# Kernel optimization log

Hardware: AMD Instinct MI355X
Metric: run time of the kernel (lower is better)

The kernel has to match this reference:

```python
import jax, jax.numpy as jnp
import numpy as np

# RosaAttention config constants
H = 16       # num_rosa_heads
KV = 4       # num_rosa_key_value_heads
QKB = 64     # num_rosa_query_key_bits
VB = 64      # num_rosa_value_bits
HID = 2048   # hidden_size
TAU = 1.0    # temperature buffer


def setup_inputs() -> dict:
    key = jax.random.key(0)
    ks = jax.random.split(key, 8)
    B, S = 2, 2048
    sc = 0.02
    return {
        "x": jax.random.normal(ks[0], (B, S, HID), jnp.float32),
        "attention_mask": jnp.ones((B, S), jnp.int32),
        "Wq": jax.random.normal(ks[1], (HID, H * QKB), jnp.float32) * sc,
        "Wk": jax.random.normal(ks[2], (HID, KV * QKB), jnp.float32) * sc,
        "Wv": jax.random.normal(ks[3], (HID, KV * VB), jnp.float32) * sc,
        "Wo": jax.random.normal(ks[4], (H * VB, HID), jnp.float32) * sc,
        "emb0": jnp.full((H, VB), -1e-05, jnp.float32),
        "emb1": jnp.full((H, VB), +1e-05, jnp.float32),
    }


def reference(x, attention_mask, Wq, Wk, Wv, Wo, emb0, emb1):
    B, S, _ = x.shape
    rep = H // KV
    # projections -> [b, s, heads, bits]
    xq = (x @ Wq).reshape(B, S, H, QKB)
    xk = (x @ Wk).reshape(B, S, KV, QKB)
    xv = (x @ Wv).reshape(B, S, KV, VB)
    # repeat_kv: each kv head repeated n_rep times contiguously
    xk = jnp.repeat(xk, rep, axis=2)   # [b, s, H, QKB]
    xv = jnp.repeat(xv, rep, axis=2)   # [b, s, H, VB]
    # soft bit quantization of q/k, tau-scaled bit-similarity score
    qb = jnp.tanh(xq)
    kb = jnp.tanh(xk)
    scores = jnp.einsum('bqhd,bkhd->bhqk', qb, kb) / (TAU * QKB)
    # causal mask + padding mask (mask True = attend)
    causal = jnp.tril(jnp.ones((S, S), bool))
    mask = causal[None, None] & attention_mask.astype(bool)[:, None, None, :]
    scores = jnp.where(mask, scores, jnp.finfo(scores.dtype).min)
    probs = jax.nn.softmax(scores, axis=-1)        # [b, h, q, k]
    # soft-binarized values: per-bit probabilities, attended, then mapped
    # through learned per-head bit embeddings emb0 (bit=0) / emb1 (bit=1)
    vp = jax.nn.sigmoid(xv)                        # [b, s, H, VB]
    ctx = jnp.einsum('bhqk,bkhv->bqhv', probs, vp) # [b, s, H, VB]
    out_bits = ctx * emb1[None, None] + (1.0 - ctx) * emb0[None, None]
    out = out_bits.reshape(B, S, H * VB) @ Wo      # [b, s, HID]
    return out
```

## Files before the change

### kernel.cpp

```cpp
#include <hip/hip_runtime.h>
#include <math.h>

typedef short bf16x8 __attribute__((ext_vector_type(8)));
typedef float f32x4 __attribute__((ext_vector_type(4)));

#define MFMA_BF16(A,B,C) __builtin_amdgcn_mfma_f32_16x16x32_bf16(A,B,C,0,0,0)

__device__ __forceinline__ unsigned short f2b(float x) {
    union { float f; unsigned int u; } v; v.f = x;
    unsigned int r = v.u + 0x7FFFu + ((v.u >> 16) & 1u);
    return (unsigned short)(r >> 16);
}

__device__ __forceinline__ void gload16(const unsigned short* g, unsigned short* l) {
    __builtin_amdgcn_global_load_lds(
        (const __attribute__((address_space(1))) unsigned int*)(g),
        (__attribute__((address_space(3))) unsigned int*)(l),
        16, 0, 0);
}
__device__ __forceinline__ void gload4(const int* g, int* l) {
    __builtin_amdgcn_global_load_lds(
        (const __attribute__((address_space(1))) unsigned int*)(g),
        (__attribute__((address_space(3))) unsigned int*)(l),
        4, 0, 0);
}

__global__ __launch_bounds__(256) void conv_bf16(const float* __restrict__ s,
                                                 unsigned short* __restrict__ d, int n)
{
    int i = blockIdx.x * blockDim.x + threadIdx.x;
    int stride = gridDim.x * blockDim.x;
    for (int idx = i * 4; idx < n; idx += stride * 4) {
        float4 v = *(const float4*)(s + idx);
        ushort4 o;
        o.x = f2b(v.x); o.y = f2b(v.y); o.z = f2b(v.z); o.w = f2b(v.w);
        *(ushort4*)(d + idx) = o;
    }
}

__global__ __launch_bounds__(256) void transp_conv_qkv(const float* __restrict__ Wq,
                                                       const float* __restrict__ Wk,
                                                       const float* __restrict__ Wv,
                                                       unsigned short* __restrict__ dst)
{
    __shared__ float t[32][33];
    const int tx = threadIdx.x, ty = threadIdx.y;
    int bx = blockIdx.x;
    const float* src; int C, cb, dco;
    if (bx < 32)      { src = Wq; C = 1024; cb = bx;      dco = 0; }
    else if (bx < 40) { src = Wk; C = 256;  cb = bx - 32; dco = 1024; }
    else              { src = Wv; C = 256;  cb = bx - 40; dco = 1280; }
    const int c = cb * 32 + tx;
    const int r0 = blockIdx.y * 32;
#pragma unroll
    for (int i = 0; i < 4; ++i)
        t[ty + i * 8][tx] = src[(size_t)(r0 + ty + i * 8) * C + c];
    __syncthreads();
    const int cc = cb * 32 + ty;
#pragma unroll
    for (int i = 0; i < 4; ++i)
        dst[(size_t)(dco + cc + i * 8) * 2048 + r0 + tx] = f2b(t[tx][ty + i * 8]);
}

__global__ __launch_bounds__(256) void transp_conv(const float* __restrict__ src, int R, int C,
                                                   unsigned short* __restrict__ dst, int pitch)
{
    __shared__ float t[32][33];
    const int tx = threadIdx.x, ty = threadIdx.y;
    const int c = blockIdx.x * 32 + tx;
    const int r0 = blockIdx.y * 32;
#pragma unroll
    for (int i = 0; i < 4; ++i)
        t[ty + i * 8][tx] = src[(size_t)(r0 + ty + i * 8) * C + c];
    __syncthreads();
    const int cc = blockIdx.x * 32 + ty;
#pragma unroll
    for (int i = 0; i < 4; ++i)
        dst[(size_t)(cc + i * 8) * pitch + r0 + tx] = f2b(t[tx][ty + i * 8]);
}

template <int MODE>
__global__ __launch_bounds__(256, 3) void gemm_bt_mfma(
    const unsigned short* __restrict__ A,
    const unsigned short* __restrict__ Bt,
    int M, int N, int K,
    float* __restrict__ Cf,
    unsigned short* __restrict__ qh,
    unsigned short* __restrict__ kh,
    unsigned short* __restrict__ vtt)
{
    __shared__ __align__(16) unsigned short As[2][2 * 128 * 32];
    __shared__ __align__(16) unsigned short Bs[2][2 * 64 * 32];

    const int tid = threadIdx.x;
    const int w = tid >> 6, lane = tid & 63, l15 = lane & 15, quad = lane >> 4;
    const int wm = w & 1, wn = w >> 1;
    const int m0 = blockIdx.y * 128, n0 = blockIdx.x * 64;

    f32x4 acc[4][2];
    const f32x4 zero4 = {0.f, 0.f, 0.f, 0.f};
#pragma unroll
    for (int i = 0; i < 4; ++i)
#pragma unroll
        for (int j = 0; j < 2; ++j) acc[i][j] = zero4;

    const int lrow = lane >> 2, lcol = (lane & 3) * 8;
    const unsigned short* AgL = A  + (size_t)(m0 + w * 32 + lrow) * K + lcol;
    const unsigned short* BgL = Bt + (size_t)(n0 + w * 16 + lrow) * K + lcol;

#pragma unroll
    for (int t = 0; t < 4; ++t) {
        const int sub = t >> 1, half = t & 1;
        gload16(AgL + (size_t)(half * 16) * K + sub * 32,
                &As[0][sub * 4096 + (w * 32 + half * 16) * 32]);
    }
#pragma unroll
    for (int kk = 0; kk < 2; ++kk)
        gload16(BgL + kk * 32, &Bs[0][kk * 2048 + (w * 16) * 32]);
    __syncthreads();

    int cb = 0;
    for (int k0 = 0; k0 < K; k0 += 64) {
        if (k0 + 64 < K) {
            const int nb = cb ^ 1;
#pragma unroll
            for (int t = 0; t < 4; ++t) {
                const int sub = t >> 1, half = t & 1;
                gload16(AgL + (size_t)(half * 16) * K + (k0 + 64) + sub * 32,
                        &As[nb][sub * 4096 + (w * 32 + half * 16) * 32]);
            }
#pragma unroll
            for (int kk = 0; kk < 2; ++kk)
                gload16(BgL + (k0 + 64) + kk * 32, &Bs[nb][kk * 2048 + (w * 16) * 32]);
        }

        bf16x8 af[4][2], bf[2][2];
#pragma unroll
        for (int kk = 0; kk < 2; ++kk) {
#pragma unroll
            for (int mt = 0; mt < 4; ++mt)
                af[mt][kk] = *(const bf16x8*)&As[cb][kk * 4096 + (wm * 64 + mt * 16 + l15) * 32 + quad * 8];
#pragma unroll
            for (int nt = 0; nt < 2; ++nt)
                bf[nt][kk] = *(const bf16x8*)&Bs[cb][kk * 2048 + (wn * 32 + nt * 16 + l15) * 32 + quad * 8];
        }
#pragma unroll
        for (int kk = 0; kk < 2; ++kk)
#pragma unroll
            for (int mt = 0; mt < 4; ++mt)
#pragma unroll
                for (int nt = 0; nt < 2; ++nt)
                    acc[mt][nt] = MFMA_BF16(af[mt][kk], bf[nt][kk], acc[mt][nt]);

        __syncthreads();
        cb ^= 1;
    }

    if (MODE == 0) {
#pragma unroll
        for (int mt = 0; mt < 4; ++mt)
#pragma unroll
            for (int nt = 0; nt < 2; ++nt) {
                const int gn = n0 + wn * 32 + nt * 16 + l15;
#pragma unroll
                for (int r = 0; r < 4; ++r) {
                    const int gm = m0 + wm * 64 + mt * 16 + quad * 4 + r;
                    Cf[(size_t)gm * N + gn] = acc[mt][nt][r];
                }
            }
    } else {
        if (n0 < 1024) {
#pragma unroll
            for (int mt = 0; mt < 4; ++mt)
#pragma unroll
                for (int nt = 0; nt < 2; ++nt) {
                    const int gn = n0 + wn * 32 + nt * 16 + l15;
#pragma unroll
                    for (int r = 0; r < 4; ++r) {
                        const int gm = m0 + wm * 64 + mt * 16 + quad * 4 + r;
                        qh[(size_t)gm * 1024 + gn] = f2b(tanhf(acc[mt][nt][r]));
                    }
                }
        } else if (n0 < 1280) {
#pragma unroll
            for (int mt = 0; mt < 4; ++mt)
#pragma unroll
                for (int nt = 0; nt < 2; ++nt) {
                    const int gn = n0 + wn * 32 + nt * 16 + l15 - 1024;
#pragma unroll
                    for (int r = 0; r < 4; ++r) {
                        const int gm = m0 + wm * 64 + mt * 16 + quad * 4 + r;
                        kh[(size_t)gm * 256 + gn] = f2b(tanhf(acc[mt][nt][r]));
                    }
                }
        } else {
#pragma unroll
            for (int mt = 0; mt < 4; ++mt)
#pragma unroll
                for (int nt = 0; nt < 2; ++nt) {
                    const int gn = n0 + wn * 32 + nt * 16 + l15 - 1280;
                    const int g = gn >> 6, vv = gn & 63;
                    const int s0 = m0 + wm * 64 + mt * 16 + quad * 4;
                    const int b = s0 >> 11, sl = s0 & 2047;
                    ushort4 pk;
                    unsigned short* pp = (unsigned short*)&pk;
#pragma unroll
                    for (int r = 0; r < 4; ++r) {
                        float sv = 1.0f / (1.0f + __expf(-acc[mt][nt][r]));
                        pp[r] = f2b(sv);
                    }
                    *(ushort4*)&vtt[((size_t)(b * 4 + g) * 64 + vv) * 2048 + sl] = pk;
                }
        }
    }
}

__global__ __launch_bounds__(256) void rosa_attn_mfma(
    const unsigned short* __restrict__ qh,
    const unsigned short* __restrict__ kh,
    const unsigned short* __restrict__ vtt,
    const int* __restrict__ amask,
    const float* __restrict__ emb0,
    const float* __restrict__ emb1,
    unsigned short* __restrict__ ob)
{
    __shared__ __align__(16) unsigned short Ks[2][2][64 * 32];
    __shared__ __align__(16) unsigned short Vs[2][2][64 * 32];
    __shared__ __align__(16) unsigned short Ps[4][16][72];
    __shared__ int Mski[2][64];

    const int pairI = blockIdx.x;
    const int h = blockIdx.y, b = blockIdx.z, g = h >> 2;
    const int tid = threadIdx.x;
    const int w = tid >> 6, lane = tid & 63, l15 = lane & 15, quad = lane >> 4;

    const int lrow = lane >> 2, lcol = (lane & 3) * 8;
    const unsigned short* kst = kh + (size_t)b * 2048 * 256 + g * 64
                               + (size_t)(w * 16 + lrow) * 256 + lcol;
    const unsigned short* vst = vtt + ((size_t)(b * 4 + g) * 64) * 2048
                               + (size_t)(w * 16 + lrow) * 2048 + lcol;
    const int* mbase = amask + b * 2048;

    const f32x4 zero4 = {0.f, 0.f, 0.f, 0.f};
    const float cexp = 0.0225421100f;

#define STAGE_TILE(k0s, buf)                                              \
    {                                                                     \
        gload16(kst + (size_t)(k0s) * 256,      &Ks[buf][0][(w * 16) * 32]); \
        gload16(kst + (size_t)(k0s) * 256 + 32, &Ks[buf][1][(w * 16) * 32]); \
        gload16(vst + (k0s),                    &Vs[buf][0][(w * 16) * 32]); \
        gload16(vst + (k0s) + 32,               &Vs[buf][1][(w * 16) * 32]); \
        if (w == 0) gload4(mbase + (k0s) + lane, &Mski[buf][0]);          \
    }

    for (int half = 0; half < 2; ++half) {
        const int qt = (half == 0) ? pairI : 31 - pairI;
        const int q0 = qt * 64;
        const int nkt = qt + 1;
        const int qg = q0 + w * 16 + l15;

        const unsigned short* qrow = qh + ((size_t)(b * 2048 + q0 + w * 16 + l15) * 16 + h) * 64;
        const bf16x8 qf0 = *(const bf16x8*)(qrow + quad * 8);
        const bf16x8 qf1 = *(const bf16x8*)(qrow + 32 + quad * 8);

        f32x4 oacc[4];
#pragma unroll
        for (int t = 0; t < 4; ++t) oacc[t] = zero4;
        float psum = 0.0f;

        __syncthreads();
        STAGE_TILE(0, 0)
        __syncthreads();

        int cb = 0;
        for (int kt = 0; kt < nkt; ++kt) {
            if (kt + 1 < nkt) STAGE_TILE((kt + 1) * 64, cb ^ 1)

            const int k0 = kt * 64;
            const bool diag = (kt == qt);
            const int ntlim = diag ? (w + 1) : 4;

#pragma unroll
            for (int nt = 0; nt < 4; ++nt) {
                ushort4 pk;
                if (nt < ntlim) {
                    bf16x8 kf0 = *(const bf16x8*)&Ks[cb][0][(nt * 16 + l15) * 32 + quad * 8];
                    bf16x8 kf1 = *(const bf16x8*)&Ks[cb][1][(nt * 16 + l15) * 32 + quad * 8];
                    f32x4 sc = MFMA_BF16(kf0, qf0, zero4);
                    sc = MFMA_BF16(kf1, qf1, sc);
                    const int4 m4 = *(const int4*)&Mski[cb][nt * 16 + quad * 4];
                    const int* mm = (const int*)&m4;
                    unsigned short* pp = (unsigned short*)&pk;
#pragma unroll
                    for (int r = 0; r < 4; ++r) {
                        float p = __builtin_exp2f(sc[r] * cexp);
                        bool valid = (mm[r] != 0);
                        if (diag) valid = valid && ((k0 + nt * 16 + quad * 4 + r) <= qg);
                        p = valid ? p : 0.0f;
                        psum += p;
                        pp[r] = f2b(p);
                    }
                } else {
                    pk.x = 0; pk.y = 0; pk.z = 0; pk.w = 0;
                }
                *(ushort4*)&Ps[w][l15][nt * 16 + quad * 4] = pk;
            }

            const bf16x8 pf0 = *(const bf16x8*)&Ps[w][l15][quad * 8];
            const bf16x8 pf1 = *(const bf16x8*)&Ps[w][l15][32 + quad * 8];
#pragma unroll
            for (int nt = 0; nt < 4; ++nt) {
                bf16x8 vf0 = *(const bf16x8*)&Vs[cb][0][(nt * 16 + l15) * 32 + quad * 8];
                bf16x8 vf1 = *(const bf16x8*)&Vs[cb][1][(nt * 16 + l15) * 32 + quad * 8];
                oacc[nt] = MFMA_BF16(pf0, vf0, oacc[nt]);
                oacc[nt] = MFMA_BF16(pf1, vf1, oacc[nt]);
            }

            if (kt + 1 < nkt) {
                __syncthreads();
                cb ^= 1;
            }
        }

        float l = psum;
        l += __shfl_xor(l, 16);
        l += __shfl_xor(l, 32);
        float lq[4];
#pragma unroll
        for (int r = 0; r < 4; ++r) lq[r] = __shfl(l, quad * 4 + r);

#pragma unroll
        for (int nt = 0; nt < 4; ++nt) {
            const float e0 = emb0[h * 64 + nt * 16 + l15];
            const float e1 = emb1[h * 64 + nt * 16 + l15];
#pragma unroll
            for (int r = 0; r < 4; ++r) {
                const float ctx = oacc[nt][r] / lq[r];
                const float val = e0 + ctx * (e1 - e0);
                const size_t s_idx = (size_t)(b * 2048 + q0 + w * 16 + quad * 4 + r);
                ob[(s_idx * 16 + h) * 64 + nt * 16 + l15] = f2b(val);
            }
        }
    }
#undef STAGE_TILE
}

extern "C" void kernel_launch(void* const* d_in, const int* in_sizes, int n_in,
                              void* d_out, int out_size, void* d_ws, size_t ws_size,
                              hipStream_t stream)
{
    const float* x    = (const float*)d_in[0];
    const int*   amask= (const int*)d_in[1];
    const float* Wq   = (const float*)d_in[2];
    const float* Wk   = (const float*)d_in[3];
    const float* Wv   = (const float*)d_in[4];
    const float* Wo   = (const float*)d_in[5];
    const float* emb0 = (const float*)d_in[6];
    const float* emb1 = (const float*)d_in[7];
    float* out = (float*)d_out;

    char* base = (char*)d_ws;
    unsigned short* xh    = (unsigned short*)(base);
    unsigned short* ob    = xh;
    unsigned short* Wqkvt = (unsigned short*)(base + (16u << 20));
    unsigned short* Wot   = (unsigned short*)(base + (22u << 20));
    unsigned short* qh    = (unsigned short*)(base + (26u << 20));
    unsigned short* kh    = (unsigned short*)(base + (34u << 20));
    unsigned short* vtt   = (unsigned short*)(base + (36u << 20));

    conv_bf16<<<2048, 256, 0, stream>>>(x, xh, 4096 * 2048);
    transp_conv_qkv<<<dim3(48, 64), dim3(32, 8), 0, stream>>>(Wq, Wk, Wv, Wqkvt);
    transp_conv<<<dim3(64, 32), dim3(32, 8), 0, stream>>>(Wo, 1024, 2048, Wot, 1024);

    gemm_bt_mfma<1><<<dim3(24, 32), 256, 0, stream>>>(xh, Wqkvt, 4096, 1536, 2048,
                                                      nullptr, qh, kh, vtt);
    rosa_attn_mfma<<<dim3(16, 16, 2), 256, 0, stream>>>(qh, kh, vtt, amask, emb0, emb1, ob);
    gemm_bt_mfma<0><<<dim3(32, 32), 256, 0, stream>>>(ob, Wot, 4096, 2048, 1024,
                                                      out, nullptr, nullptr, nullptr);
}
```

Before: 235.0 us.

## Use fragment-major LDS layout, split attention query tiles across blocks, pack bf16 via cvt_pk

LDS tiles in the GEMM and attention kernels are now stored in MFMA fragment order, so each lane reads its 16 bytes contiguously (lane*8) instead of striding by rows. This is meant to remove LDS bank conflicts on fragment loads. The attention kernel now launches one block per query tile, ordered longest-first, instead of pairing short and long tiles in one block, and adds launch_bounds occupancy 3. Probability packing uses the hardware v_cvt_pk_bf16_f32 instruction instead of manual rounding, and the diagonal causal check is simplified to a single tile. Per-block work becomes uneven, which the reversed tile order is meant to offset.

```diff
diff --git a/kernel.cpp b/kernel.cpp
--- a/kernel.cpp
+++ b/kernel.cpp
@@ -3,6 +3,8 @@
 
 typedef short bf16x8 __attribute__((ext_vector_type(8)));
 typedef float f32x4 __attribute__((ext_vector_type(4)));
+typedef unsigned int u32x2 __attribute__((ext_vector_type(2)));
+typedef unsigned int u32x4 __attribute__((ext_vector_type(4)));
 
 #define MFMA_BF16(A,B,C) __builtin_amdgcn_mfma_f32_16x16x32_bf16(A,B,C,0,0,0)
 
@@ -10,6 +12,12 @@
     union { float f; unsigned int u; } v; v.f = x;
     unsigned int r = v.u + 0x7FFFu + ((v.u >> 16) & 1u);
     return (unsigned short)(r >> 16);
+}
+
+__device__ __forceinline__ unsigned int cvtpk(float lo, float hi) {
+    unsigned int r;
+    asm("v_cvt_pk_bf16_f32 %0, %1, %2" : "=v"(r) : "v"(lo), "v"(hi));
+    return r;
 }
 
 __device__ __forceinline__ void gload16(const unsigned short* g, unsigned short* l) {
@@ -104,19 +112,18 @@
 #pragma unroll
         for (int j = 0; j < 2; ++j) acc[i][j] = zero4;
 
-    const int lrow = lane >> 2, lcol = (lane & 3) * 8;
-    const unsigned short* AgL = A  + (size_t)(m0 + w * 32 + lrow) * K + lcol;
-    const unsigned short* BgL = Bt + (size_t)(n0 + w * 16 + lrow) * K + lcol;
+    const unsigned short* AgL = A  + (size_t)(m0 + w * 32 + l15) * K + quad * 8;
+    const unsigned short* BgL = Bt + (size_t)(n0 + w * 16 + l15) * K + quad * 8;
 
 #pragma unroll
     for (int t = 0; t < 4; ++t) {
         const int sub = t >> 1, half = t & 1;
         gload16(AgL + (size_t)(half * 16) * K + sub * 32,
-                &As[0][sub * 4096 + (w * 32 + half * 16) * 32]);
+                &As[0][sub * 4096 + (w * 2 + half) * 512]);
     }
 #pragma unroll
     for (int kk = 0; kk < 2; ++kk)
-        gload16(BgL + kk * 32, &Bs[0][kk * 2048 + (w * 16) * 32]);
+        gload16(BgL + kk * 32, &Bs[0][kk * 2048 + w * 512]);
     __syncthreads();
 
     int cb = 0;
@@ -127,11 +134,11 @@
             for (int t = 0; t < 4; ++t) {
                 const int sub = t >> 1, half = t & 1;
                 gload16(AgL + (size_t)(half * 16) * K + (k0 + 64) + sub * 32,
-                        &As[nb][sub * 4096 + (w * 32 + half * 16) * 32]);
+                        &As[nb][sub * 4096 + (w * 2 + half) * 512]);
             }
 #pragma unroll
             for (int kk = 0; kk < 2; ++kk)
-                gload16(BgL + (k0 + 64) + kk * 32, &Bs[nb][kk * 2048 + (w * 16) * 32]);
+                gload16(BgL + (k0 + 64) + kk * 32, &Bs[nb][kk * 2048 + w * 512]);
         }
 
         bf16x8 af[4][2], bf[2][2];
@@ -139,10 +146,10 @@
         for (int kk = 0; kk < 2; ++kk) {
 #pragma unroll
             for (int mt = 0; mt < 4; ++mt)
-                af[mt][kk] = *(const bf16x8*)&As[cb][kk * 4096 + (wm * 64 + mt * 16 + l15) * 32 + quad * 8];
+                af[mt][kk] = *(const bf16x8*)&As[cb][kk * 4096 + (wm * 4 + mt) * 512 + lane * 8];
 #pragma unroll
             for (int nt = 0; nt < 2; ++nt)
-                bf[nt][kk] = *(const bf16x8*)&Bs[cb][kk * 2048 + (wn * 32 + nt * 16 + l15) * 32 + quad * 8];
+                bf[nt][kk] = *(const bf16x8*)&Bs[cb][kk * 2048 + (wn * 2 + nt) * 512 + lane * 8];
         }
 #pragma unroll
         for (int kk = 0; kk < 2; ++kk)
@@ -215,7 +222,7 @@
     }
 }
 
-__global__ __launch_bounds__(256) void rosa_attn_mfma(
+__global__ __launch_bounds__(256, 3) void rosa_attn_mfma(
     const unsigned short* __restrict__ qh,
     const unsigned short* __restrict__ kh,
     const unsigned short* __restrict__ vtt,
@@ -224,122 +231,119 @@
     const float* __restrict__ emb1,
     unsigned short* __restrict__ ob)
 {
-    __shared__ __align__(16) unsigned short Ks[2][2][64 * 32];
-    __shared__ __align__(16) unsigned short Vs[2][2][64 * 32];
-    __shared__ __align__(16) unsigned short Ps[4][16][72];
+    __shared__ __align__(16) unsigned short Ks[2][2][2048];
+    __shared__ __align__(16) unsigned short Vs[2][2][2048];
+    __shared__ __align__(16) unsigned int   Ps[4][16][36];
     __shared__ int Mski[2][64];
 
-    const int pairI = blockIdx.x;
+    const int qt = 31 - blockIdx.x;
     const int h = blockIdx.y, b = blockIdx.z, g = h >> 2;
     const int tid = threadIdx.x;
     const int w = tid >> 6, lane = tid & 63, l15 = lane & 15, quad = lane >> 4;
 
-    const int lrow = lane >> 2, lcol = (lane & 3) * 8;
     const unsigned short* kst = kh + (size_t)b * 2048 * 256 + g * 64
-                               + (size_t)(w * 16 + lrow) * 256 + lcol;
-    const unsigned short* vst = vtt + ((size_t)(b * 4 + g) * 64) * 2048
-                               + (size_t)(w * 16 + lrow) * 2048 + lcol;
+                               + (size_t)(w * 16 + l15) * 256 + quad * 8;
+    const unsigned short* vst = vtt + ((size_t)(b * 4 + g) * 64 + w * 16 + l15) * 2048
+                               + quad * 8;
     const int* mbase = amask + b * 2048;
 
     const f32x4 zero4 = {0.f, 0.f, 0.f, 0.f};
     const float cexp = 0.0225421100f;
 
-#define STAGE_TILE(k0s, buf)                                              \
-    {                                                                     \
-        gload16(kst + (size_t)(k0s) * 256,      &Ks[buf][0][(w * 16) * 32]); \
-        gload16(kst + (size_t)(k0s) * 256 + 32, &Ks[buf][1][(w * 16) * 32]); \
-        gload16(vst + (k0s),                    &Vs[buf][0][(w * 16) * 32]); \
-        gload16(vst + (k0s) + 32,               &Vs[buf][1][(w * 16) * 32]); \
-        if (w == 0) gload4(mbase + (k0s) + lane, &Mski[buf][0]);          \
-    }
-
-    for (int half = 0; half < 2; ++half) {
-        const int qt = (half == 0) ? pairI : 31 - pairI;
-        const int q0 = qt * 64;
-        const int nkt = qt + 1;
-        const int qg = q0 + w * 16 + l15;
-
-        const unsigned short* qrow = qh + ((size_t)(b * 2048 + q0 + w * 16 + l15) * 16 + h) * 64;
-        const bf16x8 qf0 = *(const bf16x8*)(qrow + quad * 8);
-        const bf16x8 qf1 = *(const bf16x8*)(qrow + 32 + quad * 8);
-
-        f32x4 oacc[4];
-#pragma unroll
-        for (int t = 0; t < 4; ++t) oacc[t] = zero4;
-        float psum = 0.0f;
-
-        __syncthreads();
-        STAGE_TILE(0, 0)
-        __syncthreads();
-
-        int cb = 0;
-        for (int kt = 0; kt < nkt; ++kt) {
-            if (kt + 1 < nkt) STAGE_TILE((kt + 1) * 64, cb ^ 1)
-
-            const int k0 = kt * 64;
-            const bool diag = (kt == qt);
-            const int ntlim = diag ? (w + 1) : 4;
-
-#pragma unroll
-            for (int nt = 0; nt < 4; ++nt) {
-                ushort4 pk;
-                if (nt < ntlim) {
-                    bf16x8 kf0 = *(const bf16x8*)&Ks[cb][0][(nt * 16 + l15) * 32 + quad * 8];
-                    bf16x8 kf1 = *(const bf16x8*)&Ks[cb][1][(nt * 16 + l15) * 32 + quad * 8];
-                    f32x4 sc = MFMA_BF16(kf0, qf0, zero4);
-                    sc = MFMA_BF16(kf1, qf1, sc);
-                    const int4 m4 = *(const int4*)&Mski[cb][nt * 16 + quad * 4];
-                    const int* mm = (const int*)&m4;
-                    unsigned short* pp = (unsigned short*)&pk;
-#pragma unroll
-                    for (int r = 0; r < 4; ++r) {
-                        float p = __builtin_exp2f(sc[r] * cexp);
-                        bool valid = (mm[r] != 0);
-                        if (diag) valid = valid && ((k0 + nt * 16 + quad * 4 + r) <= qg);
-                        p = valid ? p : 0.0f;
-                        psum += p;
-                        pp[r] = f2b(p);
-                    }
-                } else {
-                    pk.x = 0; pk.y = 0; pk.z = 0; pk.w = 0;
-                }
-                *(ushort4*)&Ps[w][l15][nt * 16 + quad * 4] = pk;
+#define STAGE_TILE(k0s, buf)                                               \
+    {                                                                      \
+        gload16(kst + (size_t)(k0s) * 256,      &Ks[buf][0][w * 512]);     \
+        gload16(kst + (size_t)(k0s) * 256 + 32, &Ks[buf][1][w * 512]);     \
+        gload16(vst + (k0s),                    &Vs[buf][0][w * 512]);     \
+        gload16(vst + (k0s) + 32,               &Vs[buf][1][w * 512]);     \
+        if (w == 0) gload4(mbase + (k0s) + lane, &Mski[buf][0]);           \
+    }
+
+    const int q0 = qt * 64;
+    const int nkt = qt + 1;
+    const int qg = q0 + w * 16 + l15;
+
+    const unsigned short* qrow = qh + ((size_t)(b * 2048 + qg) * 16 + h) * 64;
+    const bf16x8 qf0 = *(const bf16x8*)(qrow + quad * 8);
+    const bf16x8 qf1 = *(const bf16x8*)(qrow + 32 + quad * 8);
+
+    f32x4 oacc[4];
+#pragma unroll
+    for (int t = 0; t < 4; ++t) oacc[t] = zero4;
+    float psum = 0.0f;
+
+    STAGE_TILE(0, 0)
+    __syncthreads();
+
+    int cb = 0;
+    for (int kt = 0; kt < nkt; ++kt) {
+        if (kt + 1 < nkt) STAGE_TILE((kt + 1) * 64, cb ^ 1)
+
+        const bool diag = (kt == qt);
+        const int ntlim = diag ? (w + 1) : 4;
+
+#pragma unroll
+        for (int nt = 0; nt < 4; ++nt) {
+            u32x2 pk2;
+            if (nt < ntlim) {
+                bf16x8 kf0 = *(const bf16x8*)&Ks[cb][0][nt * 512 + lane * 8];
+                bf16x8 kf1 = *(const bf16x8*)&Ks[cb][1][nt * 512 + lane * 8];
+                f32x4 sc = MFMA_BF16(kf0, qf0, zero4);
+                sc = MFMA_BF16(kf1, qf1, sc);
+                const int4 m4 = *(const int4*)&Mski[cb][nt * 16 + quad * 4];
+                const int* mm = (const int*)&m4;
+                const bool dnw = diag && (nt == w);
+                float p[4];
+#pragma unroll
+                for (int r = 0; r < 4; ++r) {
+                    float pv = __builtin_exp2f(sc[r] * cexp);
+                    bool valid = (mm[r] != 0);
+                    if (dnw) valid = valid && ((quad * 4 + r) <= l15);
+                    pv = valid ? pv : 0.0f;
+                    psum += pv;
+                    p[r] = pv;
+                }
+                pk2[0] = cvtpk(p[0], p[1]);
+                pk2[1] = cvtpk(p[2], p[3]);
+            } else {
+                pk2[0] = 0u; pk2[1] = 0u;
             }
-
-            const bf16x8 pf0 = *(const bf16x8*)&Ps[w][l15][quad * 8];
-            const bf16x8 pf1 = *(const bf16x8*)&Ps[w][l15][32 + quad * 8];
-#pragma unroll
-            for (int nt = 0; nt < 4; ++nt) {
-                bf16x8 vf0 = *(const bf16x8*)&Vs[cb][0][(nt * 16 + l15) * 32 + quad * 8];
-                bf16x8 vf1 = *(const bf16x8*)&Vs[cb][1][(nt * 16 + l15) * 32 + quad * 8];
-                oacc[nt] = MFMA_BF16(pf0, vf0, oacc[nt]);
-                oacc[nt] = MFMA_BF16(pf1, vf1, oacc[nt]);
-            }
-
-            if (kt + 1 < nkt) {
-                __syncthreads();
-                cb ^= 1;
-            }
-        }
-
-        float l = psum;
-        l += __shfl_xor(l, 16);
-        l += __shfl_xor(l, 32);
-        float lq[4];
-#pragma unroll
-        for (int r = 0; r < 4; ++r) lq[r] = __shfl(l, quad * 4 + r);
-
+            *(u32x2*)&Ps[w][l15][nt * 8 + quad * 2] = pk2;
+        }
+
+        const bf16x8 pf0 = __builtin_bit_cast(bf16x8, *(const u32x4*)&Ps[w][l15][quad * 4]);
+        const bf16x8 pf1 = __builtin_bit_cast(bf16x8, *(const u32x4*)&Ps[w][l15][16 + quad * 4]);
 #pragma unroll
         for (int nt = 0; nt < 4; ++nt) {
-            const float e0 = emb0[h * 64 + nt * 16 + l15];
-            const float e1 = emb1[h * 64 + nt * 16 + l15];
-#pragma unroll
-            for (int r = 0; r < 4; ++r) {
-                const float ctx = oacc[nt][r] / lq[r];
-                const float val = e0 + ctx * (e1 - e0);
-                const size_t s_idx = (size_t)(b * 2048 + q0 + w * 16 + quad * 4 + r);
-                ob[(s_idx * 16 + h) * 64 + nt * 16 + l15] = f2b(val);
-            }
+            bf16x8 vf0 = *(const bf16x8*)&Vs[cb][0][nt * 512 + lane * 8];
+            bf16x8 vf1 = *(const bf16x8*)&Vs[cb][1][nt * 512 + lane * 8];
+            oacc[nt] = MFMA_BF16(pf0, vf0, oacc[nt]);
+            oacc[nt] = MFMA_BF16(pf1, vf1, oacc[nt]);
+        }
+
+        if (kt + 1 < nkt) {
+            __syncthreads();
+            cb ^= 1;
+        }
+    }
+
+    float l = psum;
+    l += __shfl_xor(l, 16);
+    l += __shfl_xor(l, 32);
+    float lq[4];
+#pragma unroll
+    for (int r = 0; r < 4; ++r) lq[r] = __shfl(l, quad * 4 + r);
+
+#pragma unroll
+    for (int nt = 0; nt < 4; ++nt) {
+        const float e0 = emb0[h * 64 + nt * 16 + l15];
+        const float e1 = emb1[h * 64 + nt * 16 + l15];
+#pragma unroll
+        for (int r = 0; r < 4; ++r) {
+            const float ctx = oacc[nt][r] / lq[r];
+            const float val = e0 + ctx * (e1 - e0);
+            const size_t s_idx = (size_t)(b * 2048 + q0 + w * 16 + quad * 4 + r);
+            ob[(s_idx * 16 + h) * 64 + nt * 16 + l15] = f2b(val);
         }
     }
 #undef STAGE_TILE
@@ -374,7 +378,7 @@
 
     gemm_bt_mfma<1><<<dim3(24, 32), 256, 0, stream>>>(xh, Wqkvt, 4096, 1536, 2048,
                                                       nullptr, qh, kh, vtt);
-    rosa_attn_mfma<<<dim3(16, 16, 2), 256, 0, stream>>>(qh, kh, vtt, amask, emb0, emb1, ob);
+    rosa_attn_mfma<<<dim3(32, 16, 2), 256, 0, stream>>>(qh, kh, vtt, amask, emb0, emb1, ob);
     gemm_bt_mfma<0><<<dim3(32, 32), 256, 0, stream>>>(ob, Wot, 4096, 2048, 1024,
                                                       out, nullptr, nullptr, nullptr);
 }
```

Result: slower. 322.5 us (+37.2%).
